# Kernel optimization log

Hardware: AMD Instinct MI355X
Metric: run time of the kernel (lower is better)

The kernel has to match this reference:

```python
import jax, jax.numpy as jnp
import numpy as np

N_NODES = 50000
N_EDGES = 1250000
D_NODE = 64
D_EDGE = 16
D_HID = 64


def setup_inputs() -> dict:
    key = jax.random.key(0)
    ks = jax.random.split(key, 12)

    def lin(k, din, dout):
        kw, kb = jax.random.split(k)
        # lecun_normal-style init (flax Linear default kernel init)
        w = jax.random.normal(kw, (din, dout), dtype=jnp.float32) / np.sqrt(din)
        b = jnp.zeros((dout,), dtype=jnp.float32)
        return w, b

    node_features = jax.random.normal(ks[0], (N_NODES, D_NODE), dtype=jnp.float32)
    edge_features = jax.random.normal(ks[1], (N_EDGES, D_EDGE), dtype=jnp.float32)
    edge_index = jax.random.randint(ks[2], (2, N_EDGES), 0, N_NODES, dtype=jnp.int64 if jax.config.jax_enable_x64 else jnp.int32)

    w_m1, b_m1 = lin(ks[3], D_NODE + D_EDGE, D_HID)
    w_m2, b_m2 = lin(ks[4], D_HID, D_HID)
    w_u1, b_u1 = lin(ks[5], D_NODE + D_HID, D_HID)
    w_u2, b_u2 = lin(ks[6], D_HID, D_HID)

    return {
        "node_features": node_features,
        "edge_features": edge_features,
        "edge_index": edge_index,
        "w_m1": w_m1, "b_m1": b_m1,
        "w_m2": w_m2, "b_m2": b_m2,
        "w_u1": w_u1, "b_u1": b_u1,
        "w_u2": w_u2, "b_u2": b_u2,
    }


def reference(node_features, edge_features, edge_index,
              w_m1, b_m1, w_m2, b_m2, w_u1, b_u1, w_u2, b_u2):
    num_nodes = node_features.shape[0]
    src, dst = edge_index[0], edge_index[1]

    # gather source node features per edge: [E, D_NODE]
    source_features = node_features[src]
    # message MLP: [E, D_NODE+D_EDGE] -> relu -> [E, D_HID]
    msg_in = jnp.concatenate([source_features, edge_features], axis=-1)
    messages = jax.nn.relu(msg_in @ w_m1 + b_m1) @ w_m2 + b_m2

    # sum aggregation to destination nodes: [N, D_HID]
    aggregated = jax.ops.segment_sum(messages, dst, num_segments=num_nodes)

    # update MLP: [N, D_NODE+D_HID] -> relu -> [N, D_HID]
    upd_in = jnp.concatenate([node_features, aggregated], axis=-1)
    return jax.nn.relu(upd_in @ w_u1 + b_u1) @ w_u2 + b_u2
```

## Files before the change

### kernel.cpp

```cpp
#include <hip/hip_runtime.h>
#include <cstdio>


#define TPB 256

__global__ __launch_bounds__(TPB)
void GraphMessagePassing_5952824672257_kernel(
    const float* __restrict__ nodef,
    const float* __restrict__ edgef,
    const int*   __restrict__ eidx,
    const float* __restrict__ w1,
    const float* __restrict__ b1,
    const float* __restrict__ w2,
    const float* __restrict__ b2,
    float* __restrict__ agg,
    int n_edges, int n_nodes)
{
    __shared__ float HB[64][65];
    __shared__ int   SI[64];
    __shared__ int   DI[64];
    float* __restrict__ Xf = &HB[0][0];

    const int tid  = threadIdx.x;
    const int lane = tid & 63;
    const int wch  = __builtin_amdgcn_readfirstlane(tid >> 6) * 16;

    const long base = (long)blockIdx.x * 64;

    if (tid < 64) {
        long e  = base + tid;
        long ec = (e < n_edges) ? e : (long)n_edges - 1;
        if (ec < 0) ec = 0;
        int s  = eidx[ec];
        int dd = eidx[(size_t)n_edges + ec];
        SI[tid] = ((unsigned)s  < (unsigned)n_nodes) ? s  : 0;
        DI[tid] = ((unsigned)dd < (unsigned)n_nodes) ? dd : 0;
    }
    __syncthreads();

    const int r  = tid & 15;
    const int e0 = tid >> 4;
    int se[4];
    #pragma unroll
    for (int i = 0; i < 4; ++i) se[i] = SI[e0 + i * 16];

    int    xoff4[4];
    size_t goff4[4];
    #pragma unroll
    for (int i = 0; i < 4; ++i) {
        int flat = i * 256 + tid;
        int e = flat >> 4, rr = flat & 15;
        long ee = base + e;
        if (ee >= n_edges) ee = n_edges - 1;
        if (ee < 0) ee = 0;
        xoff4[i] = rr * 66 + e;
        goff4[i] = (size_t)ee * 16 + rr;
    }

    float h[16];
    #pragma unroll
    for (int c = 0; c < 16; ++c) h[c] = b1[wch + c];

    float pf[4];
    #pragma unroll
    for (int i = 0; i < 4; ++i) pf[i] = nodef[(size_t)se[i] * 64 + r];
    #pragma unroll
    for (int i = 0; i < 4; ++i) Xf[r * 66 + e0 + i * 16] = pf[i];
    #pragma unroll
    for (int i = 0; i < 4; ++i) pf[i] = nodef[(size_t)se[i] * 64 + 16 + r];
    __syncthreads();

    #pragma unroll
    for (int kc = 0; kc < 5; ++kc) {
        const int cur = kc & 1;
        #pragma unroll 4
        for (int r2 = 0; r2 < 16; ++r2) {
            const float xk = Xf[cur * 1056 + r2 * 66 + lane];
            const float* __restrict__ wr = w1 + (kc * 16 + r2) * 64 + wch;
            #pragma unroll
            for (int c = 0; c < 16; ++c) h[c] = fmaf(xk, wr[c], h[c]);
        }
        if (kc < 4) {
            if (kc == 3) {
                #pragma unroll
                for (int i = 0; i < 4; ++i)
                    Xf[(cur ^ 1) * 1056 + xoff4[i]] = pf[i];
            } else {
                #pragma unroll
                for (int i = 0; i < 4; ++i)
                    Xf[(cur ^ 1) * 1056 + r * 66 + e0 + i * 16] = pf[i];
            }
            if (kc == 2) {
                #pragma unroll
                for (int i = 0; i < 4; ++i) pf[i] = edgef[goff4[i]];
            } else if (kc < 2) {
                #pragma unroll
                for (int i = 0; i < 4; ++i)
                    pf[i] = nodef[(size_t)se[i] * 64 + (kc + 2) * 16 + r];
            }
            __syncthreads();
        }
    }
    __syncthreads();

    #pragma unroll
    for (int c = 0; c < 16; ++c) HB[lane][wch + c] = fmaxf(h[c], 0.f);
    __syncthreads();

    float m[16];
    #pragma unroll
    for (int c = 0; c < 16; ++c) m[c] = b2[wch + c];
    #pragma unroll 4
    for (int t = 0; t < 64; ++t) {
        const float xt = HB[lane][t];
        const float* __restrict__ wr = w2 + t * 64 + wch;
        #pragma unroll
        for (int c = 0; c < 16; ++c) m[c] = fmaf(xt, wr[c], m[c]);
    }
    __syncthreads();

    #pragma unroll
    for (int c = 0; c < 16; ++c) HB[lane][wch + c] = m[c];
    __syncthreads();

    const int oc  = lane & 15;
    const int er4 = lane >> 4;
    #pragma unroll
    for (int g = 0; g < 16; ++g) {
        const int le = g * 4 + er4;
        const int dg = DI[le];
        const float v = HB[le][wch + oc];
        if (base + le < n_edges)
            atomicAdd(agg + (size_t)dg * 64 + wch + oc, v);
    }
}

__global__ __launch_bounds__(TPB)
void node_mlp_coop(
    const float* __restrict__ nodef,
    const float* __restrict__ agg,
    const float* __restrict__ w1,
    const float* __restrict__ b1,
    const float* __restrict__ w2,
    const float* __restrict__ b2,
    float* __restrict__ out,
    int n_nodes)
{
    __shared__ float HB[64][65];
    float* __restrict__ Xf = &HB[0][0];

    const int tid  = threadIdx.x;
    const int lane = tid & 63;
    const int wch  = __builtin_amdgcn_readfirstlane(tid >> 6) * 16;

    const long base = (long)blockIdx.x * 64;

    const int r  = tid & 15;
    const int e0 = tid >> 4;
    size_t rows[4];
    #pragma unroll
    for (int i = 0; i < 4; ++i) {
        long row = base + e0 + i * 16;
        if (row >= n_nodes) row = n_nodes - 1;
        if (row < 0) row = 0;
        rows[i] = (size_t)row * 64;
    }

    float h[16];
    #pragma unroll
    for (int c = 0; c < 16; ++c) h[c] = b1[wch + c];

    float pf[4];
    #pragma unroll
    for (int i = 0; i < 4; ++i) pf[i] = nodef[rows[i] + r];
    #pragma unroll
    for (int i = 0; i < 4; ++i) Xf[r * 66 + e0 + i * 16] = pf[i];
    #pragma unroll
    for (int i = 0; i < 4; ++i) pf[i] = nodef[rows[i] + 16 + r];
    __syncthreads();

    #pragma unroll
    for (int kc = 0; kc < 8; ++kc) {
        const int cur = kc & 1;
        #pragma unroll 4
        for (int r2 = 0; r2 < 16; ++r2) {
            const float xk = Xf[cur * 1056 + r2 * 66 + lane];
            const float* __restrict__ wr = w1 + (kc * 16 + r2) * 64 + wch;
            #pragma unroll
            for (int c = 0; c < 16; ++c) h[c] = fmaf(xk, wr[c], h[c]);
        }
        if (kc < 7) {
            #pragma unroll
            for (int i = 0; i < 4; ++i)
                Xf[(cur ^ 1) * 1056 + r * 66 + e0 + i * 16] = pf[i];
            if (kc < 6) {
                const float* __restrict__ src = (kc + 2 < 4) ? nodef : agg;
                const int ko = ((kc + 2) & 3) * 16;
                #pragma unroll
                for (int i = 0; i < 4; ++i) pf[i] = src[rows[i] + ko + r];
            }
            __syncthreads();
        }
    }
    __syncthreads();

    #pragma unroll
    for (int c = 0; c < 16; ++c) HB[lane][wch + c] = fmaxf(h[c], 0.f);
    __syncthreads();

    float m[16];
    #pragma unroll
    for (int c = 0; c < 16; ++c) m[c] = b2[wch + c];
    #pragma unroll 4
    for (int t = 0; t < 64; ++t) {
        const float xt = HB[lane][t];
        const float* __restrict__ wr = w2 + t * 64 + wch;
        #pragma unroll
        for (int c = 0; c < 16; ++c) m[c] = fmaf(xt, wr[c], m[c]);
    }
    __syncthreads();

    #pragma unroll
    for (int c = 0; c < 16; ++c) HB[lane][wch + c] = m[c];
    __syncthreads();

    const int oc  = lane & 15;
    const int er4 = lane >> 4;
    #pragma unroll
    for (int g = 0; g < 16; ++g) {
        const int le = g * 4 + er4;
        const float v = HB[le][wch + oc];
        if (base + le < n_nodes)
            out[(size_t)(base + le) * 64 + wch + oc] = v;
    }
}

extern "C" void kernel_launch(void* const* d_in, const int* in_sizes, int n_in,
                              void* d_out, int out_size, void* d_ws, size_t ws_size,
                              hipStream_t stream) {
    const float* nodef = (const float*)d_in[0];
    const float* edgef = (const float*)d_in[1];
    const int*   eidx  = (const int*)d_in[2];
    const float* w_m1  = (const float*)d_in[3];
    const float* b_m1  = (const float*)d_in[4];
    const float* w_m2  = (const float*)d_in[5];
    const float* b_m2  = (const float*)d_in[6];
    const float* w_u1  = (const float*)d_in[7];
    const float* b_u1  = (const float*)d_in[8];
    const float* w_u2  = (const float*)d_in[9];
    const float* b_u2  = (const float*)d_in[10];
    float* out = (float*)d_out;

    const int n_nodes = out_size / 64;
    const int n_edges = in_sizes[2] / 2;
    if (n_edges <= 0 || n_nodes <= 0) return;

    fprintf(stderr, "[KL] f32 4-wave-coop dbuf E=%d N=%d ws=%zu\n",
            n_edges, n_nodes, ws_size);
    fflush(stderr);

    float* agg = (float*)d_ws;
    hipMemsetAsync(agg, 0, (size_t)n_nodes * 64 * sizeof(float), stream);

    const int blocks_e = (n_edges + 63) / 64;
    GraphMessagePassing_5952824672257_kernel<<<blocks_e, TPB, 0, stream>>>(
        nodef, edgef, eidx, w_m1, b_m1, w_m2, b_m2, agg, n_edges, n_nodes);

    const int blocks_n = (n_nodes + 63) / 64;
    node_mlp_coop<<<blocks_n, TPB, 0, stream>>>(
        nodef, agg, w_u1, b_u1, w_u2, b_u2, out, n_nodes);

    hipError_t le = hipGetLastError();
    fprintf(stderr, "[KL] last=%d(%s)\n", (int)le, hipGetErrorName(le));
    fflush(stderr);
}
```

Baseline: 465.0 us.

## Run edge message MLP on MFMA with split-f16 hi/lo operands

Replaces the scalar FP32 FMA edge-message MLP with MFMA 16x16x32 f16 instructions. Each fp32 value is split into a high and a low f16 part, and three MFMAs per tile approximate fp32 accuracy. New pre-pass kernels convert the node features and transposed weights into hi/lo f16 buffers held in the workspace, and edge features are split on the fly. The aim is to move the dominant edge GEMM work off vector ALUs. The cost is extra conversion kernels, more workspace traffic, and some precision loss from dropping the lo*lo term.

```diff
diff --git a/kernel.cpp b/kernel.cpp
--- a/kernel.cpp
+++ b/kernel.cpp
@@ -2,138 +2,180 @@
 #include <cstdio>
 
 
+typedef _Float16 f16;
+typedef f16  f16x8 __attribute__((ext_vector_type(8)));
+typedef f16  f16x4 __attribute__((ext_vector_type(4)));
+typedef float f32x4 __attribute__((ext_vector_type(4)));
+
+#define MFMA16(a, b, c) __builtin_amdgcn_mfma_f32_16x16x32_f16(a, b, c, 0, 0, 0)
+
+__global__ void conv_features(const float* __restrict__ x,
+                              f16* __restrict__ xh, f16* __restrict__ xl,
+                              int n4) {
+    int i = blockIdx.x * blockDim.x + threadIdx.x;
+    if (i >= n4) return;
+    float4 v = ((const float4*)x)[i];
+    float vv[4] = {v.x, v.y, v.z, v.w};
+    f16x4 hi, lo;
+    #pragma unroll
+    for (int j = 0; j < 4; ++j) {
+        f16 h = (f16)vv[j];
+        hi[j] = h;
+        lo[j] = (f16)(vv[j] - (float)h);
+    }
+    ((f16x4*)xh)[i] = hi;
+    ((f16x4*)xl)[i] = lo;
+}
+
+__global__ void conv_weights(const float* __restrict__ w1,
+                             const float* __restrict__ w2,
+                             f16* __restrict__ w1th, f16* __restrict__ w1tl,
+                             f16* __restrict__ w2th, f16* __restrict__ w2tl) {
+    int idx = blockIdx.x * blockDim.x + threadIdx.x;
+    if (idx < 64 * 96) {
+        int c = idx / 96, k = idx % 96;
+        float v = (k < 80) ? w1[k * 64 + c] : 0.f;
+        f16 h = (f16)v;
+        w1th[c * 96 + k] = h;
+        w1tl[c * 96 + k] = (f16)(v - (float)h);
+    } else if (idx < 64 * 96 + 64 * 64) {
+        int t = idx - 64 * 96;
+        int c = t / 64, k = t % 64;
+        float v = w2[k * 64 + c];
+        f16 h = (f16)v;
+        w2th[c * 64 + k] = h;
+        w2tl[c * 64 + k] = (f16)(v - (float)h);
+    }
+}
+
+__global__ __launch_bounds__(256)
+void GraphMessagePassing_5952824672257_kernel(
+    const f16* __restrict__ nh, const f16* __restrict__ nl,
+    const float* __restrict__ edgef,
+    const int*  __restrict__ eidx,
+    const f16* __restrict__ w1th, const f16* __restrict__ w1tl,
+    const f16* __restrict__ w2th, const f16* __restrict__ w2tl,
+    const float* __restrict__ b1, const float* __restrict__ b2,
+    float* __restrict__ agg, int n_edges, int n_nodes)
+{
+    __shared__ f16 Hhi[64 * 72];
+    __shared__ f16 Hlo[64 * 72];
+
+    const int lane = threadIdx.x & 63;
+    const int wid  = threadIdx.x >> 6;
+    const int r16  = lane & 15;
+    const int g    = lane >> 4;
+    const long base = (long)blockIdx.x * 64 + wid * 16;
+
+    long es = base + r16;
+    if (es >= n_edges) es = n_edges - 1;
+    int s = eidx[es];
+    if ((unsigned)s >= (unsigned)n_nodes) s = 0;
+
+    int  dstv[4];
+    bool val[4];
+    #pragma unroll
+    for (int reg = 0; reg < 4; ++reg) {
+        long ee = base + g * 4 + reg;
+        val[reg] = ee < n_edges;
+        long ec = val[reg] ? ee : n_edges - 1;
+        int d = eidx[(size_t)n_edges + ec];
+        if ((unsigned)d >= (unsigned)n_nodes) d = 0;
+        dstv[reg] = d;
+    }
+
+    f32x4 acc[4] = {{0.f,0.f,0.f,0.f},{0.f,0.f,0.f,0.f},
+                    {0.f,0.f,0.f,0.f},{0.f,0.f,0.f,0.f}};
+
+    #pragma unroll
+    for (int kt = 0; kt < 2; ++kt) {
+        const int k0 = kt * 32 + g * 8;
+        f16x8 ahi = *(const f16x8*)&nh[(size_t)s * 64 + k0];
+        f16x8 alo = *(const f16x8*)&nl[(size_t)s * 64 + k0];
+        #pragma unroll
+        for (int nt = 0; nt < 4; ++nt) {
+            const int c = nt * 16 + r16;
+            f16x8 bhi = *(const f16x8*)&w1th[c * 96 + k0];
+            f16x8 blo = *(const f16x8*)&w1tl[c * 96 + k0];
+            acc[nt] = MFMA16(ahi, bhi, acc[nt]);
+            acc[nt] = MFMA16(ahi, blo, acc[nt]);
+            acc[nt] = MFMA16(alo, bhi, acc[nt]);
+        }
+    }
+    {
+        f16x8 ahi = {}; f16x8 alo = {};
+        if (g < 2) {
+            const float* ep = edgef + (size_t)es * 16 + g * 8;
+            float4 v0 = *(const float4*)(ep);
+            float4 v1 = *(const float4*)(ep + 4);
+            float xv[8] = {v0.x, v0.y, v0.z, v0.w, v1.x, v1.y, v1.z, v1.w};
+            #pragma unroll
+            for (int j = 0; j < 8; ++j) {
+                f16 h = (f16)xv[j];
+                ahi[j] = h;
+                alo[j] = (f16)(xv[j] - (float)h);
+            }
+        }
+        const int k0 = 64 + g * 8;
+        #pragma unroll
+        for (int nt = 0; nt < 4; ++nt) {
+            const int c = nt * 16 + r16;
+            f16x8 bhi = *(const f16x8*)&w1th[c * 96 + k0];
+            f16x8 blo = *(const f16x8*)&w1tl[c * 96 + k0];
+            acc[nt] = MFMA16(ahi, bhi, acc[nt]);
+            acc[nt] = MFMA16(ahi, blo, acc[nt]);
+            acc[nt] = MFMA16(alo, bhi, acc[nt]);
+        }
+    }
+
+    const int ebase = wid * 16 + g * 4;
+    #pragma unroll
+    for (int nt = 0; nt < 4; ++nt) {
+        const int ch = nt * 16 + r16;
+        const float bv = b1[ch];
+        #pragma unroll
+        for (int reg = 0; reg < 4; ++reg) {
+            float h = fmaxf(acc[nt][reg] + bv, 0.f);
+            f16 hh = (f16)h;
+            Hhi[(ebase + reg) * 72 + ch] = hh;
+            Hlo[(ebase + reg) * 72 + ch] = (f16)(h - (float)hh);
+        }
+    }
+    __syncthreads();
+
+    f32x4 acc2[4] = {{0.f,0.f,0.f,0.f},{0.f,0.f,0.f,0.f},
+                     {0.f,0.f,0.f,0.f},{0.f,0.f,0.f,0.f}};
+    const int arow = wid * 16 + r16;
+    #pragma unroll
+    for (int kt = 0; kt < 2; ++kt) {
+        const int k0 = kt * 32 + g * 8;
+        f16x8 ahi = *(const f16x8*)&Hhi[arow * 72 + k0];
+        f16x8 alo = *(const f16x8*)&Hlo[arow * 72 + k0];
+        #pragma unroll
+        for (int nt = 0; nt < 4; ++nt) {
+            const int c = nt * 16 + r16;
+            f16x8 bhi = *(const f16x8*)&w2th[c * 64 + k0];
+            f16x8 blo = *(const f16x8*)&w2tl[c * 64 + k0];
+            acc2[nt] = MFMA16(ahi, bhi, acc2[nt]);
+            acc2[nt] = MFMA16(ahi, blo, acc2[nt]);
+            acc2[nt] = MFMA16(alo, bhi, acc2[nt]);
+        }
+    }
+
+    #pragma unroll
+    for (int nt = 0; nt < 4; ++nt) {
+        const int ch = nt * 16 + r16;
+        const float bv = b2[ch];
+        #pragma unroll
+        for (int reg = 0; reg < 4; ++reg) {
+            if (val[reg])
+                atomicAdd(agg + (size_t)dstv[reg] * 64 + ch,
+                          acc2[nt][reg] + bv);
+        }
+    }
+}
+
 #define TPB 256
-
-__global__ __launch_bounds__(TPB)
-void GraphMessagePassing_5952824672257_kernel(
-    const float* __restrict__ nodef,
-    const float* __restrict__ edgef,
-    const int*   __restrict__ eidx,
-    const float* __restrict__ w1,
-    const float* __restrict__ b1,
-    const float* __restrict__ w2,
-    const float* __restrict__ b2,
-    float* __restrict__ agg,
-    int n_edges, int n_nodes)
-{
-    __shared__ float HB[64][65];
-    __shared__ int   SI[64];
-    __shared__ int   DI[64];
-    float* __restrict__ Xf = &HB[0][0];
-
-    const int tid  = threadIdx.x;
-    const int lane = tid & 63;
-    const int wch  = __builtin_amdgcn_readfirstlane(tid >> 6) * 16;
-
-    const long base = (long)blockIdx.x * 64;
-
-    if (tid < 64) {
-        long e  = base + tid;
-        long ec = (e < n_edges) ? e : (long)n_edges - 1;
-        if (ec < 0) ec = 0;
-        int s  = eidx[ec];
-        int dd = eidx[(size_t)n_edges + ec];
-        SI[tid] = ((unsigned)s  < (unsigned)n_nodes) ? s  : 0;
-        DI[tid] = ((unsigned)dd < (unsigned)n_nodes) ? dd : 0;
-    }
-    __syncthreads();
-
-    const int r  = tid & 15;
-    const int e0 = tid >> 4;
-    int se[4];
-    #pragma unroll
-    for (int i = 0; i < 4; ++i) se[i] = SI[e0 + i * 16];
-
-    int    xoff4[4];
-    size_t goff4[4];
-    #pragma unroll
-    for (int i = 0; i < 4; ++i) {
-        int flat = i * 256 + tid;
-        int e = flat >> 4, rr = flat & 15;
-        long ee = base + e;
-        if (ee >= n_edges) ee = n_edges - 1;
-        if (ee < 0) ee = 0;
-        xoff4[i] = rr * 66 + e;
-        goff4[i] = (size_t)ee * 16 + rr;
-    }
-
-    float h[16];
-    #pragma unroll
-    for (int c = 0; c < 16; ++c) h[c] = b1[wch + c];
-
-    float pf[4];
-    #pragma unroll
-    for (int i = 0; i < 4; ++i) pf[i] = nodef[(size_t)se[i] * 64 + r];
-    #pragma unroll
-    for (int i = 0; i < 4; ++i) Xf[r * 66 + e0 + i * 16] = pf[i];
-    #pragma unroll
-    for (int i = 0; i < 4; ++i) pf[i] = nodef[(size_t)se[i] * 64 + 16 + r];
-    __syncthreads();
-
-    #pragma unroll
-    for (int kc = 0; kc < 5; ++kc) {
-        const int cur = kc & 1;
-        #pragma unroll 4
-        for (int r2 = 0; r2 < 16; ++r2) {
-            const float xk = Xf[cur * 1056 + r2 * 66 + lane];
-            const float* __restrict__ wr = w1 + (kc * 16 + r2) * 64 + wch;
-            #pragma unroll
-            for (int c = 0; c < 16; ++c) h[c] = fmaf(xk, wr[c], h[c]);
-        }
-        if (kc < 4) {
-            if (kc == 3) {
-                #pragma unroll
-                for (int i = 0; i < 4; ++i)
-                    Xf[(cur ^ 1) * 1056 + xoff4[i]] = pf[i];
-            } else {
-                #pragma unroll
-                for (int i = 0; i < 4; ++i)
-                    Xf[(cur ^ 1) * 1056 + r * 66 + e0 + i * 16] = pf[i];
-            }
-            if (kc == 2) {
-                #pragma unroll
-                for (int i = 0; i < 4; ++i) pf[i] = edgef[goff4[i]];
-            } else if (kc < 2) {
-                #pragma unroll
-                for (int i = 0; i < 4; ++i)
-                    pf[i] = nodef[(size_t)se[i] * 64 + (kc + 2) * 16 + r];
-            }
-            __syncthreads();
-        }
-    }
-    __syncthreads();
-
-    #pragma unroll
-    for (int c = 0; c < 16; ++c) HB[lane][wch + c] = fmaxf(h[c], 0.f);
-    __syncthreads();
-
-    float m[16];
-    #pragma unroll
-    for (int c = 0; c < 16; ++c) m[c] = b2[wch + c];
-    #pragma unroll 4
-    for (int t = 0; t < 64; ++t) {
-        const float xt = HB[lane][t];
-        const float* __restrict__ wr = w2 + t * 64 + wch;
-        #pragma unroll
-        for (int c = 0; c < 16; ++c) m[c] = fmaf(xt, wr[c], m[c]);
-    }
-    __syncthreads();
-
-    #pragma unroll
-    for (int c = 0; c < 16; ++c) HB[lane][wch + c] = m[c];
-    __syncthreads();
-
-    const int oc  = lane & 15;
-    const int er4 = lane >> 4;
-    #pragma unroll
-    for (int g = 0; g < 16; ++g) {
-        const int le = g * 4 + er4;
-        const int dg = DI[le];
-        const float v = HB[le][wch + oc];
-        if (base + le < n_edges)
-            atomicAdd(agg + (size_t)dg * 64 + wch + oc, v);
-    }
-}
 
 __global__ __launch_bounds__(TPB)
 void node_mlp_coop(
@@ -255,16 +297,31 @@
     const int n_edges = in_sizes[2] / 2;
     if (n_edges <= 0 || n_nodes <= 0) return;
 
-    fprintf(stderr, "[KL] f32 4-wave-coop dbuf E=%d N=%d ws=%zu\n",
-            n_edges, n_nodes, ws_size);
+    char* wsb = (char*)d_ws;
+    float* agg = (float*)wsb;
+    size_t o = ((size_t)n_nodes * 64 * 4 + 255) & ~(size_t)255;
+    f16* nh = (f16*)(wsb + o); o += (size_t)n_nodes * 64 * 2;
+    f16* nl = (f16*)(wsb + o); o += (size_t)n_nodes * 64 * 2;
+    f16* w1th = (f16*)(wsb + o); o += 64 * 96 * 2;
+    f16* w1tl = (f16*)(wsb + o); o += 64 * 96 * 2;
+    f16* w2th = (f16*)(wsb + o); o += 64 * 64 * 2;
+    f16* w2tl = (f16*)(wsb + o); o += 64 * 64 * 2;
+
+    fprintf(stderr, "[KL] mfma-f16split E=%d N=%d ws=%zu used=%zu\n",
+            n_edges, n_nodes, ws_size, o);
     fflush(stderr);
 
-    float* agg = (float*)d_ws;
     hipMemsetAsync(agg, 0, (size_t)n_nodes * 64 * sizeof(float), stream);
 
+    const int n4 = n_nodes * 64 / 4;
+    conv_features<<<(n4 + 255) / 256, 256, 0, stream>>>(nodef, nh, nl, n4);
+    conv_weights<<<(64 * 96 + 64 * 64 + 255) / 256, 256, 0, stream>>>(
+        w_m1, w_m2, w1th, w1tl, w2th, w2tl);
+
     const int blocks_e = (n_edges + 63) / 64;
-    GraphMessagePassing_5952824672257_kernel<<<blocks_e, TPB, 0, stream>>>(
-        nodef, edgef, eidx, w_m1, b_m1, w_m2, b_m2, agg, n_edges, n_nodes);
+    GraphMessagePassing_5952824672257_kernel<<<blocks_e, 256, 0, stream>>>(
+        nh, nl, edgef, eidx, w1th, w1tl, w2th, w2tl, b_m1, b_m2,
+        agg, n_edges, n_nodes);
 
     const int blocks_n = (n_nodes + 63) / 64;
     node_mlp_coop<<<blocks_n, TPB, 0, stream>>>(
```

New measurement: 532.4 us. +14.5%, slower.
